# Optimization experiments

Hardware: AMD Instinct MI355X
Metric: run time of the kernel (lower is better)

The kernel has to match this reference:

```python
import jax, jax.numpy as jnp
import numpy as np

B, N, C, H = 32, 197, 768, 12
D = C // H  # head dim = 64


def setup_inputs() -> dict:
    key = jax.random.key(0)
    ks = jax.random.split(key, 5)
    std = 0.02
    x = jax.random.normal(ks[0], (B, N, C), dtype=jnp.float32)
    w_qkv = jax.random.normal(ks[1], (C, 3 * C), dtype=jnp.float32) * std
    w_proj = jax.random.normal(ks[2], (C, C), dtype=jnp.float32) * std
    b_proj = jnp.zeros((C,), dtype=jnp.float32)
    # 1x1 convs over the head axis of the attention map (Conv2d(H,H,1,bias=False))
    w_conv_l = jax.random.normal(ks[3], (H, H), dtype=jnp.float32) * std + jnp.eye(H, dtype=jnp.float32)
    w_conv_w = jax.random.normal(ks[4], (H, H), dtype=jnp.float32) * std + jnp.eye(H, dtype=jnp.float32)
    return {"x": x, "w_qkv": w_qkv, "w_proj": w_proj, "b_proj": b_proj,
            "w_conv_l": w_conv_l, "w_conv_w": w_conv_w}


def reference(x, w_qkv, w_proj, b_proj, w_conv_l, w_conv_w):
    b, n, c = x.shape
    h, d = H, c // H
    scale = d ** (-0.5)
    qkv = (x @ w_qkv).reshape(b, n, 3, h, d).transpose(2, 0, 3, 1, 4)  # [3,B,H,N,D]
    q, k, v = qkv[0], qkv[1], qkv[2]
    # value_map branch (control_output.need_value_map=True)
    value_map = jax.nn.softmax(jnp.einsum('bhnd,bhmd->bhnm', v, v) * scale, axis=-1)
    # scaled QK^T
    attn = jnp.einsum('bhnd,bhmd->bhnm', q * scale, k)  # [B,H,N,N]
    attention_scores = attn  # need_attn_score=True (captured pre-conv)
    # conv_l: 1x1 conv mixing heads
    attn = jnp.einsum('oh,bhnm->bonm', w_conv_l, attn)
    attention_probs = jax.nn.softmax(attn, axis=-1)  # need_attn_prob=True
    # conv_w: 1x1 conv mixing heads on the probabilities
    attn_w = jnp.einsum('oh,bhnm->bonm', w_conv_w, attention_probs)
    out = jnp.einsum('bhnm,bhmd->bhnd', attn_w, v)  # [B,H,N,D]
    out = out.transpose(0, 2, 1, 3).reshape(b, n, c)
    attention_output = out @ w_proj + b_proj
    return attention_output, attention_scores, attention_probs, value_map
```

## Files before the change

### kernel.cpp

```cpp
#include <hip/hip_runtime.h>
#include <cmath>

#define B_ 32
#define N_ 197
#define C_ 768
#define H_ 12
#define D_ 64
#define M_ (B_*N_)
#define MPAD_ 6400
#define K3_ (3*C_)
#define NN_ (N_*N_)
#define BH_ (B_*H_)
#define NP_ 208
#define KP_ 224
#define VTS_ 256
#define SCALE 0.125f

typedef __bf16 bf16x8 __attribute__((ext_vector_type(8)));
typedef __bf16 bf16x4 __attribute__((ext_vector_type(4)));
typedef float  f32x4  __attribute__((ext_vector_type(4)));
typedef float  f32x4u __attribute__((ext_vector_type(4), aligned(4)));

__device__ __forceinline__ void gl_lds16(const void* g, void* l) {
    __builtin_amdgcn_global_load_lds(
        (const __attribute__((address_space(1))) void*)g,
        (__attribute__((address_space(3))) void*)l,
        16, 0, 0);
}

__global__ __launch_bounds__(256) void cast_x_kernel(const float* __restrict__ X,
        __bf16* __restrict__ Xb) {
    const long long i = ((long long)blockIdx.x * 256 + threadIdx.x) * 4;
    if (i >= (long long)MPAD_ * 768) return;
    bf16x4 o;
    if (i < (long long)M_ * 768) {
        float4 f = *(const float4*)&X[i];
        o.x = (__bf16)f.x; o.y = (__bf16)f.y; o.z = (__bf16)f.z; o.w = (__bf16)f.w;
    } else {
        o.x = o.y = o.z = o.w = (__bf16)0.f;
    }
    *(bf16x4*)&Xb[i] = o;
}

__global__ __launch_bounds__(256) void transpose_cast(const float* __restrict__ W,
        __bf16* __restrict__ Wt, int R, int Ccols) {
    __shared__ float t[32][33];
    const int c0 = blockIdx.x * 32;
    const int r0 = blockIdx.y * 32;
    const int tx = threadIdx.x & 31, ty = threadIdx.x >> 5;
    #pragma unroll
    for (int i = ty; i < 32; i += 8)
        t[i][tx] = W[(size_t)(r0 + i) * Ccols + c0 + tx];
    __syncthreads();
    #pragma unroll
    for (int i = ty; i < 32; i += 8)
        Wt[(size_t)(c0 + i) * R + r0 + tx] = (__bf16)t[tx][i];
}

__global__ __launch_bounds__(256) void mfma_qkv(const __bf16* __restrict__ Xb,
        const __bf16* __restrict__ Wt, __bf16* __restrict__ q,
        __bf16* __restrict__ k, __bf16* __restrict__ v) {
    __shared__ __bf16 As[128*32];
    __shared__ __bf16 Bs[128*32];
    const int tid = threadIdx.x;
    const int wv = tid >> 6, ln = tid & 63;
    const int R0 = blockIdx.x * 128;
    const int C0 = blockIdx.y * 128;
    const int wm = wv >> 1, wn = wv & 1;
    const int arow = ln >> 2, akg = ln & 3;
    f32x4 acc[4][4] = {};
    for (int k0 = 0; k0 < 768; k0 += 32) {
        __syncthreads();
        #pragma unroll
        for (int s = 0; s < 2; s++) {
            const int seg = wv + s*4;
            const int row = seg*16 + arow;
            gl_lds16(Xb + (size_t)(R0 + row)*768 + k0 + akg*8,
                     (char*)As + seg*1024 + ln*16);
            gl_lds16(Wt + (size_t)(C0 + row)*768 + k0 + akg*8,
                     (char*)Bs + seg*1024 + ln*16);
        }
        __syncthreads();
        bf16x8 af[4], bfr[4];
        #pragma unroll
        for (int t = 0; t < 4; t++) {
            af[t]  = *(const bf16x8*)((const char*)As +
                        (wm*64 + t*16 + (ln & 15))*64 + (ln >> 4)*16);
            bfr[t] = *(const bf16x8*)((const char*)Bs +
                        (wn*64 + t*16 + (ln & 15))*64 + (ln >> 4)*16);
        }
        #pragma unroll
        for (int i = 0; i < 4; i++)
            #pragma unroll
            for (int j = 0; j < 4; j++)
                acc[i][j] = __builtin_amdgcn_mfma_f32_16x16x32_bf16(
                                af[i], bfr[j], acc[i][j], 0, 0, 0);
    }
    const int lr = (ln >> 4) * 4;
    const int lc = ln & 15;
    #pragma unroll
    for (int j = 0; j < 4; j++) {
        const int c = C0 + wn*64 + j*16 + lc;
        const int which = c / 768;
        const int rem = c - which*768;
        const int h = rem >> 6, d = rem & 63;
        __bf16* dst = (which == 0) ? q : ((which == 1) ? k : v);
        #pragma unroll
        for (int i = 0; i < 4; i++) {
            #pragma unroll
            for (int rr = 0; rr < 4; rr++) {
                const int r = R0 + wm*64 + i*16 + lr + rr;
                if (r < M_) {
                    const int bb = r / N_, n = r - bb*N_;
                    dst[(((size_t)(bb*H_ + h))*N_ + n)*64 + d] =
                        (__bf16)acc[i][j][rr];
                }
            }
        }
    }
}

__global__ __launch_bounds__(256) void mfma_proj(const __bf16* __restrict__ Ab,
        const __bf16* __restrict__ Wt, const float* __restrict__ bias,
        float* __restrict__ Y) {
    __shared__ __bf16 As[128*32];
    __shared__ __bf16 Bs[128*32];
    const int tid = threadIdx.x;
    const int wv = tid >> 6, ln = tid & 63;
    const int R0 = blockIdx.x * 128;
    const int C0 = blockIdx.y * 128;
    const int wm = wv >> 1, wn = wv & 1;
    const int arow = ln >> 2, akg = ln & 3;
    f32x4 acc[4][4] = {};
    for (int k0 = 0; k0 < 768; k0 += 32) {
        __syncthreads();
        #pragma unroll
        for (int s = 0; s < 2; s++) {
            const int seg = wv + s*4;
            const int row = seg*16 + arow;
            gl_lds16(Ab + (size_t)(R0 + row)*768 + k0 + akg*8,
                     (char*)As + seg*1024 + ln*16);
            gl_lds16(Wt + (size_t)(C0 + row)*768 + k0 + akg*8,
                     (char*)Bs + seg*1024 + ln*16);
        }
        __syncthreads();
        bf16x8 af[4], bfr[4];
        #pragma unroll
        for (int t = 0; t < 4; t++) {
            af[t]  = *(const bf16x8*)((const char*)As +
                        (wm*64 + t*16 + (ln & 15))*64 + (ln >> 4)*16);
            bfr[t] = *(const bf16x8*)((const char*)Bs +
                        (wn*64 + t*16 + (ln & 15))*64 + (ln >> 4)*16);
        }
        #pragma unroll
        for (int i = 0; i < 4; i++)
            #pragma unroll
            for (int j = 0; j < 4; j++)
                acc[i][j] = __builtin_amdgcn_mfma_f32_16x16x32_bf16(
                                af[i], bfr[j], acc[i][j], 0, 0, 0);
    }
    const int lr = (ln >> 4) * 4;
    const int lc = ln & 15;
    #pragma unroll
    for (int j = 0; j < 4; j++) {
        const int c = C0 + wn*64 + j*16 + lc;
        const float bv = bias[c];
        #pragma unroll
        for (int i = 0; i < 4; i++) {
            #pragma unroll
            for (int rr = 0; rr < 4; rr++) {
                const int r = R0 + wm*64 + i*16 + lr + rr;
                if (r < M_) Y[(size_t)r*768 + c] = acc[i][j][rr] + bv;
            }
        }
    }
}

__global__ __launch_bounds__(256) void qkt_vvt(const __bf16* __restrict__ Q,
        const __bf16* __restrict__ Km, const __bf16* __restrict__ V,
        float* __restrict__ S, float* __restrict__ VM) {
    __shared__ __bf16 Al[NP_*64];
    __shared__ __bf16 Bl[NP_*64];
    const int tid = threadIdx.x;
    const int w = tid >> 6, L = tid & 63;
    const int lm = L & 15, lg = L >> 4;
    if (blockIdx.x < BH_) {
        const int bh = blockIdx.x;
        const __bf16* Qb = Q  + (size_t)bh*N_*D_;
        const __bf16* Kb = Km + (size_t)bh*N_*D_;
        for (int i = tid*8; i < NP_*64; i += 2048) {
            const int row = i >> 6;
            const int di = (i & ~63) | ((((i >> 3) & 7) ^ (row & 7)) << 3);
            bf16x8 z = {};
            *(bf16x8*)&Al[di] = (row < N_) ? *(const bf16x8*)&Qb[i] : z;
            *(bf16x8*)&Bl[di] = (row < N_) ? *(const bf16x8*)&Kb[i] : z;
        }
        __syncthreads();
        const bool isw0 = (w == 0);
        int nts[4];
        nts[0] = w; nts[1] = w + 4; nts[2] = w + 8; nts[3] = isw0 ? 12 : w;
        bf16x8 qf0[4], qf1[4];
        #pragma unroll
        for (int t = 0; t < 4; t++) {
            const int qr = nts[t]*16 + lm;
            qf0[t] = *(const bf16x8*)&Al[qr*64 + ((lg ^ (qr & 7)) << 3)];
            qf1[t] = *(const bf16x8*)&Al[qr*64 + (((4 + lg) ^ (qr & 7)) << 3)];
        }
        for (int mt = 0; mt < 13; mt++) {
            const int kr = mt*16 + lm;
            const bf16x8 k0 = *(const bf16x8*)&Bl[kr*64 + ((lg ^ (kr & 7)) << 3)];
            const bf16x8 k1 = *(const bf16x8*)&Bl[kr*64 + (((4 + lg) ^ (kr & 7)) << 3)];
            const int m0 = mt*16 + lg*4;
            #pragma unroll
            for (int t = 0; t < 4; t++) {
                f32x4 acc = {};
                acc = __builtin_amdgcn_mfma_f32_16x16x32_bf16(k0, qf0[t], acc, 0, 0, 0);
                acc = __builtin_amdgcn_mfma_f32_16x16x32_bf16(k1, qf1[t], acc, 0, 0, 0);
                const int n = nts[t]*16 + lm;
                if ((t < 3 || isw0) && n < N_) {
                    float* Srow = S + ((size_t)bh*N_ + n)*N_;
                    if (m0 + 3 < N_) {
                        f32x4 st;
                        #pragma unroll
                        for (int r = 0; r < 4; r++) st[r] = acc[r] * SCALE;
                        *(f32x4u*)&Srow[m0] = st;
                    } else {
                        #pragma unroll
                        for (int r = 0; r < 4; r++)
                            if (m0 + r < N_) Srow[m0 + r] = acc[r] * SCALE;
                    }
                }
            }
        }
    } else {
        const int bh = blockIdx.x - BH_;
        const __bf16* Vb = V + (size_t)bh*N_*D_;
        for (int i = tid*8; i < NP_*64; i += 2048) {
            const int row = i >> 6;
            const int di = (i & ~63) | ((((i >> 3) & 7) ^ (row & 7)) << 3);
            bf16x8 z = {};
            *(bf16x8*)&Al[di] = (row < N_) ? *(const bf16x8*)&Vb[i] : z;
        }
        __syncthreads();
        for (int nt = w; nt < 13; nt += 4) {
            const int qr = nt*16 + lm;
            const bf16x8 q0 = *(const bf16x8*)&Al[qr*64 + ((lg ^ (qr & 7)) << 3)];
            const bf16x8 q1 = *(const bf16x8*)&Al[qr*64 + (((4 + lg) ^ (qr & 7)) << 3)];
            f32x4 acc[13];
            for (int mt = 0; mt < 13; mt++) {
                const int kr = mt*16 + lm;
                const bf16x8 a0 = *(const bf16x8*)&Al[kr*64 + ((lg ^ (kr & 7)) << 3)];
                const bf16x8 a1 = *(const bf16x8*)&Al[kr*64 + (((4 + lg) ^ (kr & 7)) << 3)];
                f32x4 a = {};
                a = __builtin_amdgcn_mfma_f32_16x16x32_bf16(a0, q0, a, 0, 0, 0);
                a = __builtin_amdgcn_mfma_f32_16x16x32_bf16(a1, q1, a, 0, 0, 0);
                acc[mt] = a;
            }
            #pragma unroll
            for (int mt = 0; mt < 13; mt++)
                #pragma unroll
                for (int r = 0; r < 4; r++) acc[mt][r] *= SCALE;
            #pragma unroll
            for (int r = 0; r < 4; r++)
                if (192 + lg*4 + r >= N_) acc[12][r] = -1e30f;
            float mx = -1e30f;
            #pragma unroll
            for (int mt = 0; mt < 13; mt++)
                #pragma unroll
                for (int r = 0; r < 4; r++) mx = fmaxf(mx, acc[mt][r]);
            mx = fmaxf(mx, __shfl_xor(mx, 16));
            mx = fmaxf(mx, __shfl_xor(mx, 32));
            float sm = 0.f;
            #pragma unroll
            for (int mt = 0; mt < 13; mt++)
                #pragma unroll
                for (int r = 0; r < 4; r++) {
                    const float e = __expf(acc[mt][r] - mx);
                    acc[mt][r] = e;
                    sm += e;
                }
            sm += __shfl_xor(sm, 16);
            sm += __shfl_xor(sm, 32);
            const float inv = 1.f / sm;
            const int n = qr;
            if (n < N_) {
                float* Vrow = VM + ((size_t)bh*N_ + n)*N_;
                #pragma unroll
                for (int mt = 0; mt < 12; mt++) {
                    f32x4 st;
                    #pragma unroll
                    for (int r = 0; r < 4; r++) st[r] = acc[mt][r] * inv;
                    *(f32x4u*)&Vrow[mt*16 + lg*4] = st;
                }
                #pragma unroll
                for (int r = 0; r < 4; r++) {
                    const int m = 192 + lg*4 + r;
                    if (m < N_) Vrow[m] = acc[12][r] * inv;
                }
            }
        }
    }
}

__global__ __launch_bounds__(256) void convl_convw(const float* __restrict__ SC,
        const float* __restrict__ wl, const float* __restrict__ ww,
        float* __restrict__ PR, __bf16* __restrict__ AW) {
    __shared__ float raw[12*200];
    __shared__ float mixed[12*200];
    __shared__ float wls[144];
    __shared__ float wws[144];
    const int tid = threadIdx.x;
    const int b = blockIdx.x / N_;
    const int n = blockIdx.x - b * N_;
    if (tid < 144) { wls[tid] = wl[tid]; wws[tid] = ww[tid]; }
    for (int i = tid; i < 12*N_; i += 256) {
        int h = i / N_, m = i - h*N_;
        raw[h*200 + m] = SC[(((size_t)(b*12 + h))*N_ + n)*N_ + m];
    }
    __syncthreads();
    for (int i = tid; i < 12*N_; i += 256) {
        int o = i / N_, m = i - o*N_;
        float s = 0.f;
        #pragma unroll
        for (int h = 0; h < 12; h++) s += wls[o*12 + h] * raw[h*200 + m];
        mixed[o*200 + m] = s;
    }
    __syncthreads();
    const int w = tid >> 6, l = tid & 63;
    for (int j = 0; j < 3; j++) {
        const int o = w*3 + j;
        float vv[4];
        float mx = -1e30f;
        #pragma unroll
        for (int c = 0; c < 4; c++) {
            int m = l + 64*c;
            vv[c] = (m < N_) ? mixed[o*200 + m] : -1e30f;
            mx = fmaxf(mx, vv[c]);
        }
        #pragma unroll
        for (int off = 32; off; off >>= 1) mx = fmaxf(mx, __shfl_xor(mx, off));
        float s = 0.f;
        #pragma unroll
        for (int c = 0; c < 4; c++) {
            int m = l + 64*c;
            if (m < N_) { vv[c] = __expf(vv[c] - mx); s += vv[c]; }
        }
        #pragma unroll
        for (int off = 32; off; off >>= 1) s += __shfl_xor(s, off);
        const float inv = 1.f / s;
        float* Prow = PR + (((size_t)(b*12 + o))*N_ + n)*N_;
        #pragma unroll
        for (int c = 0; c < 4; c++) {
            int m = l + 64*c;
            if (m < N_) {
                const float p = vv[c] * inv;
                Prow[m] = p;
                raw[o*200 + m] = p;
            }
        }
    }
    __syncthreads();
    for (int i = tid; i < 12*KP_; i += 256) {
        int o = i / KP_, m = i - o*KP_;
        float s = 0.f;
        if (m < N_) {
            #pragma unroll
            for (int h = 0; h < 12; h++) s += wws[o*12 + h] * raw[h*200 + m];
        }
        AW[((size_t)(b*12 + o)*N_ + n)*KP_ + m] = (__bf16)s;
    }
}

__global__ __launch_bounds__(256) void av_mfma(const __bf16* __restrict__ AW,
        const __bf16* __restrict__ V, __bf16* __restrict__ OP) {
    __shared__ __bf16 Vt[64*VTS_];
    const int tid = threadIdx.x, bh = blockIdx.x;
    const int w = tid >> 6, L = tid & 63;
    for (int i = tid*8; i < 64*VTS_; i += 2048) {
        bf16x8 z = {};
        *(bf16x8*)&Vt[i] = z;
    }
    __syncthreads();
    const __bf16* Vb = V + (size_t)bh*N_*D_;
    for (int i = tid*8; i < N_*D_; i += 2048) {
        const int row = i >> 6, col = i & 63;
        const bf16x8 vv = *(const bf16x8*)&Vb[i];
        #pragma unroll
        for (int j = 0; j < 8; j++) {
            const int d = col + j;
            Vt[d*VTS_ + ((((row >> 3) ^ (d & 7)) << 3) | (row & 7))] = vv[j];
        }
    }
    __syncthreads();
    const int lm = L & 15, lg = L >> 4;
    const int b = bh / H_, h = bh - b*H_;
    const __bf16* Ab = AW + (size_t)bh*N_*KP_;
    for (int rt = w; rt < 13; rt += 4) {
        int ar = rt*16 + lm;
        if (ar >= N_) ar = 0;
        f32x4 acc[4] = {};
        #pragma unroll
        for (int k0 = 0; k0 < KP_; k0 += 32) {
            const bf16x8 a = *(const bf16x8*)&Ab[(size_t)ar*KP_ + k0 + lg*8];
            #pragma unroll
            for (int ct = 0; ct < 4; ct++) {
                const int dr = ct*16 + lm;
                const bf16x8 bf = *(const bf16x8*)
                    &Vt[dr*VTS_ + ((((k0 >> 3) + lg) ^ (lm & 7)) << 3)];
                acc[ct] = __builtin_amdgcn_mfma_f32_16x16x32_bf16(
                              a, bf, acc[ct], 0, 0, 0);
            }
        }
        const int rbase = rt*16 + lg*4;
        #pragma unroll
        for (int ct = 0; ct < 4; ct++) {
            const int d = ct*16 + lm;
            #pragma unroll
            for (int r = 0; r < 4; r++) {
                const int row = rbase + r;
                if (row < N_)
                    OP[((size_t)(b*N_ + row))*C_ + h*64 + d] = (__bf16)acc[ct][r];
            }
        }
    }
}

extern "C" void kernel_launch(void* const* d_in, const int* in_sizes, int n_in,
                              void* d_out, int out_size, void* d_ws, size_t ws_size,
                              hipStream_t stream) {
    const float* x      = (const float*)d_in[0];
    const float* w_qkv  = (const float*)d_in[1];
    const float* w_proj = (const float*)d_in[2];
    const float* b_proj = (const float*)d_in[3];
    const float* w_cl   = (const float*)d_in[4];
    const float* w_cw   = (const float*)d_in[5];

    float* out    = (float*)d_out;
    float* scores = out    + (size_t)M_ * C_;
    float* probs  = scores + (size_t)BH_ * NN_;
    float* vmap   = probs  + (size_t)BH_ * NN_;

    char* base = (char*)d_ws;
    const size_t QS = (size_t)BH_ * N_ * D_;
    __bf16* q   = (__bf16*)base;
    __bf16* k   = q + QS;
    __bf16* v   = k + QS;
    __bf16* Xb  = v + QS;
    __bf16* OPb = Xb;
    __bf16* Wqt = Xb + (size_t)MPAD_*768;
    __bf16* Wpt = Wqt + (size_t)K3_*768;
    __bf16* aw  = Wpt + (size_t)768*768;

    cast_x_kernel <<<(MPAD_*768/4 + 255)/256, 256, 0, stream>>>(x, Xb);
    transpose_cast<<<dim3(72, 24),  256, 0, stream>>>(w_qkv,  Wqt, 768, K3_);
    transpose_cast<<<dim3(24, 24),  256, 0, stream>>>(w_proj, Wpt, 768, 768);

    mfma_qkv      <<<dim3(50, 18),  256, 0, stream>>>(Xb, Wqt, q, k, v);
    qkt_vvt       <<<2*BH_,         256, 0, stream>>>(q, k, v, scores, vmap);
    convl_convw   <<<M_,            256, 0, stream>>>(scores, w_cl, w_cw, probs, aw);
    av_mfma       <<<BH_,           256, 0, stream>>>(aw, v, OPb);
    mfma_proj     <<<dim3(50, 6),   256, 0, stream>>>(OPb, Wpt, b_proj, out);
}
```

Measured before the change: 388.9 us.

## Double-buffer LDS tiles in QKV/proj GEMMs and restructure head-mixing loops

The QKV and projection GEMMs now use two LDS buffers, prefetching the next K-slice via global_load_lds while MFMAs run on the current one, which leaves one barrier per iteration instead of two. The aim is to hide global-load latency behind compute, at the cost of doubling the LDS footprint per block. Separately, the convl/convw head-mixing loops now run one thread per column: each thread loads the 12 head values into registers once and computes all 12 outputs, which removes repeated LDS reads and integer divides. The AW padding zeros are written in a separate loop. With 197 columns and 256 threads, about 59 threads sit idle during the mixing loops.

```diff
diff --git a/kernel.cpp b/kernel.cpp
--- a/kernel.cpp
+++ b/kernel.cpp
@@ -60,8 +60,8 @@
 __global__ __launch_bounds__(256) void mfma_qkv(const __bf16* __restrict__ Xb,
         const __bf16* __restrict__ Wt, __bf16* __restrict__ q,
         __bf16* __restrict__ k, __bf16* __restrict__ v) {
-    __shared__ __bf16 As[128*32];
-    __shared__ __bf16 Bs[128*32];
+    __shared__ __bf16 As[2][128*32];
+    __shared__ __bf16 Bs[2][128*32];
     const int tid = threadIdx.x;
     const int wv = tid >> 6, ln = tid & 63;
     const int R0 = blockIdx.x * 128;
@@ -69,25 +69,38 @@
     const int wm = wv >> 1, wn = wv & 1;
     const int arow = ln >> 2, akg = ln & 3;
     f32x4 acc[4][4] = {};
-    for (int k0 = 0; k0 < 768; k0 += 32) {
+    #pragma unroll
+    for (int s = 0; s < 2; s++) {
+        const int seg = wv + s*4;
+        const int row = seg*16 + arow;
+        gl_lds16(Xb + (size_t)(R0 + row)*768 + akg*8,
+                 (char*)As[0] + seg*1024 + ln*16);
+        gl_lds16(Wt + (size_t)(C0 + row)*768 + akg*8,
+                 (char*)Bs[0] + seg*1024 + ln*16);
+    }
+    for (int t = 0; t < 24; t++) {
+        const int cur = t & 1;
+        asm volatile("s_waitcnt vmcnt(0)" ::: "memory");
         __syncthreads();
-        #pragma unroll
-        for (int s = 0; s < 2; s++) {
-            const int seg = wv + s*4;
-            const int row = seg*16 + arow;
-            gl_lds16(Xb + (size_t)(R0 + row)*768 + k0 + akg*8,
-                     (char*)As + seg*1024 + ln*16);
-            gl_lds16(Wt + (size_t)(C0 + row)*768 + k0 + akg*8,
-                     (char*)Bs + seg*1024 + ln*16);
-        }
-        __syncthreads();
+        if (t < 23) {
+            const int k0 = (t + 1) * 32;
+            #pragma unroll
+            for (int s = 0; s < 2; s++) {
+                const int seg = wv + s*4;
+                const int row = seg*16 + arow;
+                gl_lds16(Xb + (size_t)(R0 + row)*768 + k0 + akg*8,
+                         (char*)As[cur^1] + seg*1024 + ln*16);
+                gl_lds16(Wt + (size_t)(C0 + row)*768 + k0 + akg*8,
+                         (char*)Bs[cur^1] + seg*1024 + ln*16);
+            }
+        }
         bf16x8 af[4], bfr[4];
         #pragma unroll
-        for (int t = 0; t < 4; t++) {
-            af[t]  = *(const bf16x8*)((const char*)As +
-                        (wm*64 + t*16 + (ln & 15))*64 + (ln >> 4)*16);
-            bfr[t] = *(const bf16x8*)((const char*)Bs +
-                        (wn*64 + t*16 + (ln & 15))*64 + (ln >> 4)*16);
+        for (int f = 0; f < 4; f++) {
+            af[f]  = *(const bf16x8*)((const char*)As[cur] +
+                        (wm*64 + f*16 + (ln & 15))*64 + (ln >> 4)*16);
+            bfr[f] = *(const bf16x8*)((const char*)Bs[cur] +
+                        (wn*64 + f*16 + (ln & 15))*64 + (ln >> 4)*16);
         }
         #pragma unroll
         for (int i = 0; i < 4; i++)
@@ -123,8 +136,8 @@
 __global__ __launch_bounds__(256) void mfma_proj(const __bf16* __restrict__ Ab,
         const __bf16* __restrict__ Wt, const float* __restrict__ bias,
         float* __restrict__ Y) {
-    __shared__ __bf16 As[128*32];
-    __shared__ __bf16 Bs[128*32];
+    __shared__ __bf16 As[2][128*32];
+    __shared__ __bf16 Bs[2][128*32];
     const int tid = threadIdx.x;
     const int wv = tid >> 6, ln = tid & 63;
     const int R0 = blockIdx.x * 128;
@@ -132,25 +145,38 @@
     const int wm = wv >> 1, wn = wv & 1;
     const int arow = ln >> 2, akg = ln & 3;
     f32x4 acc[4][4] = {};
-    for (int k0 = 0; k0 < 768; k0 += 32) {
+    #pragma unroll
+    for (int s = 0; s < 2; s++) {
+        const int seg = wv + s*4;
+        const int row = seg*16 + arow;
+        gl_lds16(Ab + (size_t)(R0 + row)*768 + akg*8,
+                 (char*)As[0] + seg*1024 + ln*16);
+        gl_lds16(Wt + (size_t)(C0 + row)*768 + akg*8,
+                 (char*)Bs[0] + seg*1024 + ln*16);
+    }
+    for (int t = 0; t < 24; t++) {
+        const int cur = t & 1;
+        asm volatile("s_waitcnt vmcnt(0)" ::: "memory");
         __syncthreads();
-        #pragma unroll
-        for (int s = 0; s < 2; s++) {
-            const int seg = wv + s*4;
-            const int row = seg*16 + arow;
-            gl_lds16(Ab + (size_t)(R0 + row)*768 + k0 + akg*8,
-                     (char*)As + seg*1024 + ln*16);
-            gl_lds16(Wt + (size_t)(C0 + row)*768 + k0 + akg*8,
-                     (char*)Bs + seg*1024 + ln*16);
-        }
-        __syncthreads();
+        if (t < 23) {
+            const int k0 = (t + 1) * 32;
+            #pragma unroll
+            for (int s = 0; s < 2; s++) {
+                const int seg = wv + s*4;
+                const int row = seg*16 + arow;
+                gl_lds16(Ab + (size_t)(R0 + row)*768 + k0 + akg*8,
+                         (char*)As[cur^1] + seg*1024 + ln*16);
+                gl_lds16(Wt + (size_t)(C0 + row)*768 + k0 + akg*8,
+                         (char*)Bs[cur^1] + seg*1024 + ln*16);
+            }
+        }
         bf16x8 af[4], bfr[4];
         #pragma unroll
-        for (int t = 0; t < 4; t++) {
-            af[t]  = *(const bf16x8*)((const char*)As +
-                        (wm*64 + t*16 + (ln & 15))*64 + (ln >> 4)*16);
-            bfr[t] = *(const bf16x8*)((const char*)Bs +
-                        (wn*64 + t*16 + (ln & 15))*64 + (ln >> 4)*16);
+        for (int f = 0; f < 4; f++) {
+            af[f]  = *(const bf16x8*)((const char*)As[cur] +
+                        (wm*64 + f*16 + (ln & 15))*64 + (ln >> 4)*16);
+            bfr[f] = *(const bf16x8*)((const char*)Bs[cur] +
+                        (wn*64 + f*16 + (ln & 15))*64 + (ln >> 4)*16);
         }
         #pragma unroll
         for (int i = 0; i < 4; i++)
@@ -318,12 +344,17 @@
         raw[h*200 + m] = SC[(((size_t)(b*12 + h))*N_ + n)*N_ + m];
     }
     __syncthreads();
-    for (int i = tid; i < 12*N_; i += 256) {
-        int o = i / N_, m = i - o*N_;
-        float s = 0.f;
-        #pragma unroll
-        for (int h = 0; h < 12; h++) s += wls[o*12 + h] * raw[h*200 + m];
-        mixed[o*200 + m] = s;
+    for (int m = tid; m < N_; m += 256) {
+        float in[12];
+        #pragma unroll
+        for (int h = 0; h < 12; h++) in[h] = raw[h*200 + m];
+        #pragma unroll
+        for (int o = 0; o < 12; o++) {
+            float s = 0.f;
+            #pragma unroll
+            for (int h = 0; h < 12; h++) s += wls[o*12 + h] * in[h];
+            mixed[o*200 + m] = s;
+        }
     }
     __syncthreads();
     const int w = tid >> 6, l = tid & 63;
@@ -360,14 +391,22 @@
         }
     }
     __syncthreads();
-    for (int i = tid; i < 12*KP_; i += 256) {
-        int o = i / KP_, m = i - o*KP_;
-        float s = 0.f;
-        if (m < N_) {
-            #pragma unroll
-            for (int h = 0; h < 12; h++) s += wws[o*12 + h] * raw[h*200 + m];
-        }
-        AW[((size_t)(b*12 + o)*N_ + n)*KP_ + m] = (__bf16)s;
+    for (int m = tid; m < N_; m += 256) {
+        float in[12];
+        #pragma unroll
+        for (int h = 0; h < 12; h++) in[h] = raw[h*200 + m];
+        #pragma unroll
+        for (int o = 0; o < 12; o++) {
+            float s = 0.f;
+            #pragma unroll
+            for (int h = 0; h < 12; h++) s += wws[o*12 + h] * in[h];
+            AW[((size_t)(b*12 + o)*N_ + n)*KP_ + m] = (__bf16)s;
+        }
+    }
+    for (int i = tid; i < 12*(KP_-N_); i += 256) {
+        const int o = i / (KP_-N_);
+        const int m = N_ + i - o*(KP_-N_);
+        AW[((size_t)(b*12 + o)*N_ + n)*KP_ + m] = (__bf16)0.f;
     }
 }
 
```

New measurement: 370.8 us. 1.05x faster.
